# Kernel optimization log

Hardware: AMD Instinct MI355X
Metric: run time of the kernel (lower is better)

Reference implementation:

```python
import jax, jax.numpy as jnp
import numpy as np

NUM_HEADS = 16
HEAD_DIM = 64
EMBED_DIM = 1024
MASKED_BIAS = -10000.0


def setup_inputs() -> dict:
    key = jax.random.key(0)
    ks = jax.random.split(key, 4)
    B, S, D = 4, 1024, EMBED_DIM
    scale = 0.02
    return {
        "hidden_states": jax.random.normal(ks[0], (B, S, D), dtype=jnp.float32),
        "c_attn_w": jax.random.normal(ks[1], (D, 3 * D), dtype=jnp.float32) * scale,
        "c_attn_b": jnp.zeros((3 * D,), dtype=jnp.float32),
        "c_proj_w": jax.random.normal(ks[2], (D, D), dtype=jnp.float32) * scale,
        "c_proj_b": jnp.zeros((D,), dtype=jnp.float32),
        "affine_w": jnp.ones((D,), dtype=jnp.float32),
        "affine_b": jnp.zeros((D,), dtype=jnp.float32),
    }


def reference(hidden_states, c_attn_w, c_attn_b, c_proj_w, c_proj_b, affine_w, affine_b):
    B, S, D = hidden_states.shape
    H, Dh = NUM_HEADS, HEAD_DIM
    # c_attn (GPT2 Conv1D): x @ W + b -> [B,S,3D], split into q,k,v
    qkv = hidden_states @ c_attn_w + c_attn_b
    q, k, v = jnp.split(qkv, 3, axis=-1)
    # split heads -> [B,H,S,Dh]
    def split_heads(t):
        return t.reshape(B, S, H, Dh).transpose(0, 2, 1, 3)
    q, k, v = split_heads(q), split_heads(k), split_heads(v)
    # QK^T scaled by 1/sqrt(head_dim) (value.size(-1)**0.5)
    attn_weights = jnp.einsum("bhqd,bhkd->bhqk", q, k) / jnp.asarray(
        Dh, hidden_states.dtype) ** 0.5
    # causal mask via where with -10000 sentinel (eager GPT2 semantics)
    causal = jnp.tril(jnp.ones((S, S), dtype=bool))[None, None]
    attn_weights = jnp.where(causal, attn_weights,
                             jnp.asarray(MASKED_BIAS, attn_weights.dtype))
    attn_weights = jax.nn.softmax(attn_weights, axis=-1)
    # attn dropout = identity in eval
    attn_output = jnp.einsum("bhqk,bhkd->bhqd", attn_weights, v)
    # merge heads -> [B,S,D]
    attn_output = attn_output.transpose(0, 2, 1, 3).reshape(B, S, D)
    # c_proj (Conv1D), resid dropout identity, then affine
    attn_output = attn_output @ c_proj_w + c_proj_b
    attn_output = attn_output * affine_w + affine_b
    return attn_output
```

## Files before the change

kernel.cpp:

```cpp
#include <hip/hip_runtime.h>


typedef __attribute__((ext_vector_type(4))) float  fx4;
typedef __attribute__((ext_vector_type(4))) short  sx4;
typedef __attribute__((ext_vector_type(8))) short  sx8;
typedef __attribute__((ext_vector_type(4))) float  f32x4;
typedef __attribute__((ext_vector_type(8))) __bf16 bf16x8;

#define DEVI static __device__ __forceinline__

DEVI short f2bf(float f) {
  unsigned u = __builtin_bit_cast(unsigned, f);
  u = (u + 0x7FFFu + ((u >> 16) & 1u)) >> 16;
  return (short)u;
}

DEVI fx4 mfma16(sx8 a, sx8 b, fx4 c) {
  return __builtin_amdgcn_mfma_f32_16x16x32_bf16(
      __builtin_bit_cast(bf16x8, a), __builtin_bit_cast(bf16x8, b), c, 0, 0, 0);
}

DEVI void gl_lds16(const void* g, void* l) {
  __builtin_amdgcn_global_load_lds(
      (const __attribute__((address_space(1))) void*)g,
      (__attribute__((address_space(3))) void*)l, 16, 0, 0);
}

__global__ __launch_bounds__(256) void cast_bf16(const float* __restrict__ in,
                                                 short* __restrict__ out, int n4) {
  int i = blockIdx.x * blockDim.x + threadIdx.x;
  if (i < n4) {
    f32x4 v = *(const f32x4*)&in[(size_t)i * 4];
    sx4 o;
#pragma unroll
    for (int j = 0; j < 4; ++j) o[j] = f2bf(v[j]);
    *(sx4*)&out[(size_t)i * 4] = o;
  }
}

__global__ __launch_bounds__(256) void transpose_bf16(const float* __restrict__ in,
                                                      short* __restrict__ out,
                                                      int R, int C) {
  __shared__ float t[32][33];
  int tx = threadIdx.x & 31, ty = threadIdx.x >> 5;
  int r0 = blockIdx.y * 32, c0 = blockIdx.x * 32;
#pragma unroll
  for (int i = 0; i < 4; ++i)
    t[ty + i * 8][tx] = in[(size_t)(r0 + ty + i * 8) * C + c0 + tx];
  __syncthreads();
#pragma unroll
  for (int i = 0; i < 4; ++i)
    out[(size_t)(c0 + ty + i * 8) * R + r0 + tx] = f2bf(t[tx][ty + i * 8]);
}

__global__ __launch_bounds__(512, 2) void gemm_qkv(
    const short* __restrict__ A, const short* __restrict__ Bt,
    const float* __restrict__ bias, short* __restrict__ Qg,
    short* __restrict__ Kg, short* __restrict__ Vtg) {
  __shared__ __align__(16) short As[2][256][64];
  __shared__ __align__(16) short Bs[2][256][64];
  const int tid = threadIdx.x, lane = tid & 63, w = tid >> 6;
  const int bid = blockIdx.x;
  const int x = bid & 7, k = bid >> 3;
  const int bm = (x & 3) * 4 + (k & 3);
  const int bn = (x >> 2) * 6 + (k >> 2);
  const int wm = w >> 2, wn = w & 3;
  const int c0 = lane & 15, g = lane >> 4;
  const int lr8 = lane >> 3;
  const int ls8 = (lane & 7) ^ lr8;
  const int K = 1024;
  fx4 acc[8][4] = {};

  auto STAGE = [&](int bf, int kt) {
#pragma unroll
    for (int i = 0; i < 4; ++i) {
      int r = w * 32 + i * 8;
      gl_lds16(&A[(size_t)(bm * 256 + r + lr8) * K + kt + ls8 * 8], &As[bf][r][0]);
      gl_lds16(&Bt[(size_t)(bn * 256 + r + lr8) * K + kt + ls8 * 8], &Bs[bf][r][0]);
    }
  };

  STAGE(0, 0);
  for (int t = 0; t < 16; ++t) {
    const int bf = t & 1;
    if (t + 1 < 16) {
      STAGE(bf ^ 1, (t + 1) * 64);
      asm volatile("s_waitcnt vmcnt(8)" ::: "memory");
    } else {
      asm volatile("s_waitcnt vmcnt(0)" ::: "memory");
    }
    __builtin_amdgcn_s_barrier();

#pragma unroll
    for (int q = 0; q < 4; ++q) {
      const int m0 = (q >> 1) * 4, n0 = (q & 1) * 2;
      sx8 af[4][2], bfr[2][2];
#pragma unroll
      for (int m = 0; m < 4; ++m) {
        int row = wm * 128 + (m0 + m) * 16 + c0;
#pragma unroll
        for (int kk = 0; kk < 2; ++kk)
          af[m][kk] = *(const sx8*)&As[bf][row][((kk * 4 + g) ^ (row & 7)) * 8];
      }
#pragma unroll
      for (int n = 0; n < 2; ++n) {
        int row = wn * 64 + (n0 + n) * 16 + c0;
#pragma unroll
        for (int kk = 0; kk < 2; ++kk)
          bfr[n][kk] = *(const sx8*)&Bs[bf][row][((kk * 4 + g) ^ (row & 7)) * 8];
      }
      __builtin_amdgcn_sched_barrier(0);
      __builtin_amdgcn_s_barrier();
      __builtin_amdgcn_s_setprio(1);
#pragma unroll
      for (int kk = 0; kk < 2; ++kk)
#pragma unroll
        for (int m = 0; m < 4; ++m)
#pragma unroll
          for (int n = 0; n < 2; ++n)
            acc[m0 + m][n0 + n] = mfma16(af[m][kk], bfr[n][kk], acc[m0 + m][n0 + n]);
      __builtin_amdgcn_s_setprio(0);
      __builtin_amdgcn_s_barrier();
    }
  }

  const float SCALE_Q = 0.125f * 1.4426950408889634f;
#pragma unroll
  for (int m = 0; m < 8; ++m) {
#pragma unroll
    for (int n = 0; n < 4; ++n) {
      int col = bn * 256 + wn * 64 + n * 16 + c0;
      int row0 = bm * 256 + wm * 128 + m * 16 + g * 4;
      float bv = bias[col];
      int b = row0 >> 10, s0 = row0 & 1023;
      if (col < 1024) {
        int h = col >> 6, d = col & 63;
        size_t base = ((size_t)(b * 16 + h) * 1024) * 64 + d;
#pragma unroll
        for (int r = 0; r < 4; ++r)
          Qg[base + (size_t)(s0 + r) * 64] = f2bf((acc[m][n][r] + bv) * SCALE_Q);
      } else if (col < 2048) {
        int c = col - 1024, h = c >> 6, d = c & 63;
        size_t base = ((size_t)(b * 16 + h) * 1024) * 64 + d;
#pragma unroll
        for (int r = 0; r < 4; ++r)
          Kg[base + (size_t)(s0 + r) * 64] = f2bf(acc[m][n][r] + bv);
      } else {
        int c = col - 2048, h = c >> 6, d = c & 63;
        sx4 v;
#pragma unroll
        for (int r = 0; r < 4; ++r) v[r] = f2bf(acc[m][n][r] + bv);
        *(sx4*)&Vtg[((size_t)(b * 16 + h) * 64 + d) * 1024 + s0] = v;
      }
    }
  }
}

__global__ __launch_bounds__(512, 4) void gemm_proj(
    const short* __restrict__ A, const short* __restrict__ Bt,
    const float* __restrict__ bias, const float* __restrict__ aw,
    const float* __restrict__ ab, float* __restrict__ Out) {
  __shared__ __align__(16) short As[2][128][64];
  __shared__ __align__(16) short Bs[2][128][64];
  const int tid = threadIdx.x, lane = tid & 63, w = tid >> 6;
  const int bid = blockIdx.x;
  const int x = bid & 7, k = bid >> 3;
  const int bn = x + 0 * 8, bm = k;
  const int wm = w >> 2, wn = w & 3;
  const int c0 = lane & 15, g = lane >> 4;
  const int lr8 = lane >> 3, ls8 = (lane & 7) ^ lr8;
  const int K = 1024, N = 1024;
  fx4 acc[4][2] = {};

  auto STAGE = [&](int bf, int kt) {
#pragma unroll
    for (int i = 0; i < 2; ++i) {
      int idx = w * 2 + i;
      gl_lds16(&A[(size_t)(bm * 128 + idx * 8 + lr8) * K + kt + ls8 * 8],
               &As[bf][idx * 8][0]);
      gl_lds16(&Bt[(size_t)(bn * 128 + idx * 8 + lr8) * K + kt + ls8 * 8],
               &Bs[bf][idx * 8][0]);
    }
  };

  STAGE(0, 0);
  for (int t = 0; t < 16; ++t) {
    const int bf = t & 1;
    if (t + 1 < 16) {
      STAGE(bf ^ 1, (t + 1) * 64);
      asm volatile("s_waitcnt vmcnt(4)" ::: "memory");
    } else {
      asm volatile("s_waitcnt vmcnt(0)" ::: "memory");
    }
    __builtin_amdgcn_s_barrier();
    __builtin_amdgcn_s_setprio(1);
#pragma unroll
    for (int kk = 0; kk < 2; ++kk) {
      sx8 af[4], bfr[2];
      int sb = kk * 4 + g;
#pragma unroll
      for (int m = 0; m < 4; ++m) {
        int row = wm * 64 + m * 16 + c0;
        af[m] = *(const sx8*)&As[bf][row][(sb ^ (row & 7)) * 8];
      }
#pragma unroll
      for (int n = 0; n < 2; ++n) {
        int row = wn * 32 + n * 16 + c0;
        bfr[n] = *(const sx8*)&Bs[bf][row][(sb ^ (row & 7)) * 8];
      }
#pragma unroll
      for (int m = 0; m < 4; ++m)
#pragma unroll
        for (int n = 0; n < 2; ++n) acc[m][n] = mfma16(af[m], bfr[n], acc[m][n]);
    }
    __builtin_amdgcn_s_setprio(0);
    __builtin_amdgcn_s_barrier();
  }

#pragma unroll
  for (int m = 0; m < 4; ++m) {
#pragma unroll
    for (int n = 0; n < 2; ++n) {
      int col = bn * 128 + wn * 32 + n * 16 + c0;
      int row0 = bm * 128 + wm * 64 + m * 16 + g * 4;
      float bv = bias[col], wv = aw[col], av = ab[col];
#pragma unroll
      for (int r = 0; r < 4; ++r)
        Out[(size_t)(row0 + r) * N + col] = (acc[m][n][r] + bv) * wv + av;
    }
  }
}

__global__ __launch_bounds__(256, 4) void attn_kernel(const short* __restrict__ Qg,
                                                      const short* __restrict__ Kg,
                                                      const short* __restrict__ Vtg,
                                                      short* __restrict__ AO) {
  __shared__ __align__(16) short Ks[2][64][64];
  __shared__ __align__(16) short Vts[2][64][64];
  __shared__ __align__(16) short Ps[4][16 * 64];
  const int tid = threadIdx.x, lane = tid & 63, w = tid >> 6;
  const int bid = blockIdx.x;
  const int u = bid >> 8, v = bid & 255, bh = v >> 2, jj = v & 3;
  const int qt = (u == 0) ? jj : (u == 1) ? 7 - jj : (u == 2) ? 8 + jj : 15 - jj;
  const int b = bh >> 4, h = bh & 15;
  const int c0 = lane & 15, g = lane >> 4;
  const int lr8 = lane >> 3, ls8 = (lane & 7) ^ lr8;
  const int q0 = qt * 64 + w * 16;
  const short* Qp = Qg + (size_t)bh * 65536;
  const short* Kp = Kg + (size_t)bh * 65536;
  const short* Vp = Vtg + (size_t)bh * 65536;
  short* pbase = &Ps[w][0];
  const int s8 = (c0 & 7) * 8;

  sx8 qf[2];
#pragma unroll
  for (int kk = 0; kk < 2; ++kk)
    qf[kk] = *(const sx8*)&Qp[(size_t)(q0 + c0) * 64 + kk * 32 + g * 8];

  fx4 o[4] = {};
  float mrun = -1e30f, lrun = 0.f;
  const int q_glob = q0 + c0;

  auto STAGE = [&](int bf, int kv0) {
#pragma unroll
    for (int i = 0; i < 2; ++i) {
      int idx = w * 2 + i;
      gl_lds16(&Kp[(size_t)(kv0 + idx * 8 + lr8) * 64 + ls8 * 8], &Ks[bf][idx * 8][0]);
    }
#pragma unroll
    for (int i = 0; i < 2; ++i) {
      int idx = w * 2 + i;
      gl_lds16(&Vp[(size_t)(idx * 8 + lr8) * 1024 + kv0 + ls8 * 8], &Vts[bf][idx * 8][0]);
    }
  };

  STAGE(0, 0);
  for (int t = 0; t <= qt; ++t) {
    const int kv0 = t * 64;
    const int bf = t & 1;
    const bool more = t < qt;
    if (more) {
      STAGE(bf ^ 1, kv0 + 64);
      asm volatile("s_waitcnt vmcnt(4)" ::: "memory");
    } else {
      asm volatile("s_waitcnt vmcnt(0)" ::: "memory");
    }
    __builtin_amdgcn_s_barrier();

    fx4 st[4];
    __builtin_amdgcn_s_setprio(1);
#pragma unroll
    for (int mf = 0; mf < 4; ++mf) {
      int row = mf * 16 + c0;
      sx8 kf0 = *(const sx8*)&Ks[bf][row][(g ^ (row & 7)) * 8];
      sx8 kf1 = *(const sx8*)&Ks[bf][row][((4 + g) ^ (row & 7)) * 8];
      fx4 z = {0.f, 0.f, 0.f, 0.f};
      z = mfma16(kf0, qf[0], z);
      st[mf] = mfma16(kf1, qf[1], z);
    }
    __builtin_amdgcn_s_setprio(0);

    float pmax = -1e30f;
    if (t == qt) {
#pragma unroll
      for (int mf = 0; mf < 4; ++mf)
#pragma unroll
        for (int r = 0; r < 4; ++r) {
          int kv = kv0 + mf * 16 + g * 4 + r;
          float z = (kv > q_glob) ? -1e30f : st[mf][r];
          st[mf][r] = z;
          pmax = fmaxf(pmax, z);
        }
    } else {
#pragma unroll
      for (int mf = 0; mf < 4; ++mf)
#pragma unroll
        for (int r = 0; r < 4; ++r) pmax = fmaxf(pmax, st[mf][r]);
    }
    pmax = fmaxf(pmax, __shfl_xor(pmax, 16));
    pmax = fmaxf(pmax, __shfl_xor(pmax, 32));
    float mnew = fmaxf(mrun, pmax);
    float alpha = __builtin_amdgcn_exp2f(mrun - mnew);
    float psum = 0.f;
#pragma unroll
    for (int mf = 0; mf < 4; ++mf) {
      sx4 pv;
#pragma unroll
      for (int r = 0; r < 4; ++r) {
        float pp = __builtin_amdgcn_exp2f(st[mf][r] - mnew);
        psum += pp;
        pv[r] = f2bf(pp);
      }
      *(sx4*)&pbase[c0 * 64 + ((mf * 16 + g * 4) ^ s8)] = pv;
    }
    psum += __shfl_xor(psum, 16);
    psum += __shfl_xor(psum, 32);
    lrun = lrun * alpha + psum;
    mrun = mnew;
#pragma unroll
    for (int mf = 0; mf < 4; ++mf) o[mf] *= alpha;

    __builtin_amdgcn_s_setprio(1);
#pragma unroll
    for (int kk = 0; kk < 2; ++kk) {
      sx8 pbf = *(const sx8*)&pbase[c0 * 64 + ((kk * 32 + g * 8) ^ s8)];
#pragma unroll
      for (int mf = 0; mf < 4; ++mf) {
        int row = mf * 16 + c0;
        sx8 vaf = *(const sx8*)&Vts[bf][row][((kk * 4 + g) ^ (row & 7)) * 8];
        o[mf] = mfma16(vaf, pbf, o[mf]);
      }
    }
    __builtin_amdgcn_s_setprio(0);
    __builtin_amdgcn_s_barrier();
  }

  float inv = 1.0f / lrun;
  int q = q0 + c0;
#pragma unroll
  for (int mf = 0; mf < 4; ++mf) {
    sx4 v4;
#pragma unroll
    for (int r = 0; r < 4; ++r) v4[r] = f2bf(o[mf][r] * inv);
    int d0 = mf * 16 + g * 4;
    *(sx4*)&AO[((size_t)(b * 1024 + q)) * 1024 + h * 64 + d0] = v4;
  }
}

extern "C" void kernel_launch(void* const* d_in, const int* in_sizes, int n_in,
                              void* d_out, int out_size, void* d_ws, size_t ws_size,
                              hipStream_t stream) {
  const float* hs  = (const float*)d_in[0];
  const float* caw = (const float*)d_in[1];
  const float* cab = (const float*)d_in[2];
  const float* cpw = (const float*)d_in[3];
  const float* cpb = (const float*)d_in[4];
  const float* afw = (const float*)d_in[5];
  const float* afb = (const float*)d_in[6];
  float* out = (float*)d_out;
  char* ws = (char*)d_ws;

  short* hsb    = (short*)(ws);
  short* ao     = (short*)(ws);
  short* wqkvt  = (short*)(ws + ((size_t)8  << 20));
  short* wprojt = (short*)(ws + ((size_t)14 << 20));
  short* Qg     = (short*)(ws + ((size_t)16 << 20));
  short* Kg     = (short*)(ws + ((size_t)24 << 20));
  short* Vtg    = (short*)(ws + ((size_t)32 << 20));

  cast_bf16<<<4096, 256, 0, stream>>>(hs, hsb, 1048576);
  transpose_bf16<<<dim3(96, 32), 256, 0, stream>>>(caw, wqkvt, 1024, 3072);
  transpose_bf16<<<dim3(32, 32), 256, 0, stream>>>(cpw, wprojt, 1024, 1024);
  gemm_qkv<<<192, 512, 0, stream>>>(hsb, wqkvt, cab, Qg, Kg, Vtg);
  attn_kernel<<<1024, 256, 0, stream>>>(Qg, Kg, Vtg, ao);
  gemm_proj<<<256, 512, 0, stream>>>(ao, wprojt, cpb, afw, afb, out);
}
```

Before: 110.6 us.

## Halve QKV GEMM K-tile to 32 and drop intra-tile quadrant barriers

The QKV GEMM now stages K-slices of 32 instead of 64, halving LDS use per buffer, and uses a new XOR swizzle suited to 4 slots per row. The main loop runs 32 iterations, each loading all 8x4 fragments at once and issuing 32 MFMAs with a single barrier, instead of four quadrant phases separated by extra barriers. This is meant to cut synchronisation overhead and LDS footprint, possibly raising occupancy. In exchange it doubles the number of global-load stages and barriers per tile and raises fragment register pressure.

```diff
diff --git a/kernel.cpp b/kernel.cpp
--- a/kernel.cpp
+++ b/kernel.cpp
@@ -57,8 +57,8 @@
     const short* __restrict__ A, const short* __restrict__ Bt,
     const float* __restrict__ bias, short* __restrict__ Qg,
     short* __restrict__ Kg, short* __restrict__ Vtg) {
-  __shared__ __align__(16) short As[2][256][64];
-  __shared__ __align__(16) short Bs[2][256][64];
+  __shared__ __align__(16) short As[2][256][32];
+  __shared__ __align__(16) short Bs[2][256][32];
   const int tid = threadIdx.x, lane = tid & 63, w = tid >> 6;
   const int bid = blockIdx.x;
   const int x = bid & 7, k = bid >> 3;
@@ -66,62 +66,51 @@
   const int bn = (x >> 2) * 6 + (k >> 2);
   const int wm = w >> 2, wn = w & 3;
   const int c0 = lane & 15, g = lane >> 4;
-  const int lr8 = lane >> 3;
-  const int ls8 = (lane & 7) ^ lr8;
+  const int lr16 = lane >> 2;
+  const int xs = (lr16 ^ (lr16 >> 2)) & 3;
+  const int src_slot = (lane & 3) ^ xs;
   const int K = 1024;
   fx4 acc[8][4] = {};
 
   auto STAGE = [&](int bf, int kt) {
 #pragma unroll
-    for (int i = 0; i < 4; ++i) {
-      int r = w * 32 + i * 8;
-      gl_lds16(&A[(size_t)(bm * 256 + r + lr8) * K + kt + ls8 * 8], &As[bf][r][0]);
-      gl_lds16(&Bt[(size_t)(bn * 256 + r + lr8) * K + kt + ls8 * 8], &Bs[bf][r][0]);
+    for (int i = 0; i < 2; ++i) {
+      int ch = w * 2 + i;
+      int row = ch * 16 + lr16;
+      gl_lds16(&A[(size_t)(bm * 256 + row) * K + kt + src_slot * 8], &As[bf][ch * 16][0]);
+      gl_lds16(&Bt[(size_t)(bn * 256 + row) * K + kt + src_slot * 8], &Bs[bf][ch * 16][0]);
     }
   };
 
   STAGE(0, 0);
-  for (int t = 0; t < 16; ++t) {
+  for (int t = 0; t < 32; ++t) {
     const int bf = t & 1;
-    if (t + 1 < 16) {
-      STAGE(bf ^ 1, (t + 1) * 64);
-      asm volatile("s_waitcnt vmcnt(8)" ::: "memory");
+    if (t + 1 < 32) {
+      STAGE(bf ^ 1, (t + 1) * 32);
+      asm volatile("s_waitcnt vmcnt(4)" ::: "memory");
     } else {
       asm volatile("s_waitcnt vmcnt(0)" ::: "memory");
     }
     __builtin_amdgcn_s_barrier();
 
-#pragma unroll
-    for (int q = 0; q < 4; ++q) {
-      const int m0 = (q >> 1) * 4, n0 = (q & 1) * 2;
-      sx8 af[4][2], bfr[2][2];
-#pragma unroll
-      for (int m = 0; m < 4; ++m) {
-        int row = wm * 128 + (m0 + m) * 16 + c0;
-#pragma unroll
-        for (int kk = 0; kk < 2; ++kk)
-          af[m][kk] = *(const sx8*)&As[bf][row][((kk * 4 + g) ^ (row & 7)) * 8];
-      }
-#pragma unroll
-      for (int n = 0; n < 2; ++n) {
-        int row = wn * 64 + (n0 + n) * 16 + c0;
-#pragma unroll
-        for (int kk = 0; kk < 2; ++kk)
-          bfr[n][kk] = *(const sx8*)&Bs[bf][row][((kk * 4 + g) ^ (row & 7)) * 8];
-      }
-      __builtin_amdgcn_sched_barrier(0);
-      __builtin_amdgcn_s_barrier();
-      __builtin_amdgcn_s_setprio(1);
-#pragma unroll
-      for (int kk = 0; kk < 2; ++kk)
-#pragma unroll
-        for (int m = 0; m < 4; ++m)
-#pragma unroll
-          for (int n = 0; n < 2; ++n)
-            acc[m0 + m][n0 + n] = mfma16(af[m][kk], bfr[n][kk], acc[m0 + m][n0 + n]);
-      __builtin_amdgcn_s_setprio(0);
-      __builtin_amdgcn_s_barrier();
-    }
+    sx8 af[8], bfr[4];
+#pragma unroll
+    for (int m = 0; m < 8; ++m) {
+      int row = wm * 128 + m * 16 + c0;
+      af[m] = *(const sx8*)&As[bf][row][(g ^ ((row ^ (row >> 2)) & 3)) * 8];
+    }
+#pragma unroll
+    for (int n = 0; n < 4; ++n) {
+      int row = wn * 64 + n * 16 + c0;
+      bfr[n] = *(const sx8*)&Bs[bf][row][(g ^ ((row ^ (row >> 2)) & 3)) * 8];
+    }
+    __builtin_amdgcn_s_setprio(1);
+#pragma unroll
+    for (int m = 0; m < 8; ++m)
+#pragma unroll
+      for (int n = 0; n < 4; ++n) acc[m][n] = mfma16(af[m], bfr[n], acc[m][n]);
+    __builtin_amdgcn_s_setprio(0);
+    __builtin_amdgcn_s_barrier();
   }
 
   const float SCALE_Q = 0.125f * 1.4426950408889634f;
@@ -165,7 +154,7 @@
   const int tid = threadIdx.x, lane = tid & 63, w = tid >> 6;
   const int bid = blockIdx.x;
   const int x = bid & 7, k = bid >> 3;
-  const int bn = x + 0 * 8, bm = k;
+  const int bn = x, bm = k;
   const int wm = w >> 2, wn = w & 3;
   const int c0 = lane & 15, g = lane >> 4;
   const int lr8 = lane >> 3, ls8 = (lane & 7) ^ lr8;
```

Result: no change. 110.0 us (-0.6%).

## Restructure QKV GEMM into 4-phase half-tile pipeline with interleaved loads

Applied to the files above, without the earlier changes.

The QKV GEMM main loop is rewritten so that A and B tiles are staged in halves, one half at a time, and each half-load is issued between MFMA phases. Fragments are reused across quadrants (af reused for two n-halves, bfr kept for all four), which cuts LDS reads. Loads run up to two k-steps ahead, so global-to-LDS traffic overlaps with compute more finely. The cost is more barriers per iteration and more complex vmcnt accounting, plus a higher risk of a race between half-tile writes and reads. Barriers in the other kernels are switched to an inline asm s_barrier with a memory clobber.

```diff
diff --git a/kernel.cpp b/kernel.cpp
--- a/kernel.cpp
+++ b/kernel.cpp
@@ -8,6 +8,7 @@
 typedef __attribute__((ext_vector_type(8))) __bf16 bf16x8;
 
 #define DEVI static __device__ __forceinline__
+#define BARRIER asm volatile("s_barrier" ::: "memory")
 
 DEVI short f2bf(float f) {
   unsigned u = __builtin_bit_cast(unsigned, f);
@@ -66,62 +67,122 @@
   const int bn = (x >> 2) * 6 + (k >> 2);
   const int wm = w >> 2, wn = w & 3;
   const int c0 = lane & 15, g = lane >> 4;
-  const int lr8 = lane >> 3;
-  const int ls8 = (lane & 7) ^ lr8;
+  const int lr8 = lane >> 3, ls8 = (lane & 7) ^ lr8;
   const int K = 1024;
+  const int sw = c0 & 7;
   fx4 acc[8][4] = {};
 
-  auto STAGE = [&](int bf, int kt) {
-#pragma unroll
-    for (int i = 0; i < 4; ++i) {
-      int r = w * 32 + i * 8;
-      gl_lds16(&A[(size_t)(bm * 256 + r + lr8) * K + kt + ls8 * 8], &As[bf][r][0]);
-      gl_lds16(&Bt[(size_t)(bn * 256 + r + lr8) * K + kt + ls8 * 8], &Bs[bf][r][0]);
+  auto SA = [&](int h, int u) {
+    if (u > 15) return;
+    const int bf = u & 1;
+#pragma unroll
+    for (int i = 0; i < 2; ++i) {
+      int ch = w * 2 + i;
+      int r = (ch >> 3) * 128 + h * 64 + (ch & 7) * 8;
+      gl_lds16(&A[(size_t)(bm * 256 + r + lr8) * K + u * 64 + ls8 * 8],
+               &As[bf][r][0]);
     }
   };
-
-  STAGE(0, 0);
+  auto SB = [&](int h, int u) {
+    if (u > 15) return;
+    const int bf = u & 1;
+#pragma unroll
+    for (int i = 0; i < 2; ++i) {
+      int ch = w * 2 + i;
+      int r = (ch >> 2) * 64 + h * 32 + (ch & 3) * 8;
+      gl_lds16(&Bt[(size_t)(bn * 256 + r + lr8) * K + u * 64 + ls8 * 8],
+               &Bs[bf][r][0]);
+    }
+  };
+
+  SA(0, 0); SB(0, 0); SA(1, 0); SB(1, 0); SA(0, 1); SB(0, 1);
+  asm volatile("s_waitcnt vmcnt(0)" ::: "memory");
+  BARRIER;
+
+  sx8 af[4][2], bfr[4][2];
   for (int t = 0; t < 16; ++t) {
     const int bf = t & 1;
-    if (t + 1 < 16) {
-      STAGE(bf ^ 1, (t + 1) * 64);
-      asm volatile("s_waitcnt vmcnt(8)" ::: "memory");
-    } else {
+#pragma unroll
+    for (int mi = 0; mi < 4; ++mi) {
+      int r = wm * 128 + mi * 16 + c0;
+#pragma unroll
+      for (int kk = 0; kk < 2; ++kk)
+        af[mi][kk] = *(const sx8*)&As[bf][r][(((kk << 2) | g) ^ sw) * 8];
+    }
+#pragma unroll
+    for (int n = 0; n < 2; ++n) {
+      int r = wn * 64 + n * 16 + c0;
+#pragma unroll
+      for (int kk = 0; kk < 2; ++kk)
+        bfr[n][kk] = *(const sx8*)&Bs[bf][r][(((kk << 2) | g) ^ sw) * 8];
+    }
+    SA(1, t + 1);
+    BARRIER;
+    __builtin_amdgcn_s_setprio(1);
+#pragma unroll
+    for (int kk = 0; kk < 2; ++kk)
+#pragma unroll
+      for (int mi = 0; mi < 4; ++mi)
+#pragma unroll
+        for (int n = 0; n < 2; ++n)
+          acc[mi][n] = mfma16(af[mi][kk], bfr[n][kk], acc[mi][n]);
+    __builtin_amdgcn_s_setprio(0);
+    BARRIER;
+#pragma unroll
+    for (int n = 2; n < 4; ++n) {
+      int r = wn * 64 + n * 16 + c0;
+#pragma unroll
+      for (int kk = 0; kk < 2; ++kk)
+        bfr[n][kk] = *(const sx8*)&Bs[bf][r][(((kk << 2) | g) ^ sw) * 8];
+    }
+    SB(1, t + 1);
+    BARRIER;
+    __builtin_amdgcn_s_setprio(1);
+#pragma unroll
+    for (int kk = 0; kk < 2; ++kk)
+#pragma unroll
+      for (int mi = 0; mi < 4; ++mi)
+#pragma unroll
+        for (int n = 2; n < 4; ++n)
+          acc[mi][n] = mfma16(af[mi][kk], bfr[n][kk], acc[mi][n]);
+    __builtin_amdgcn_s_setprio(0);
+    BARRIER;
+#pragma unroll
+    for (int mi = 0; mi < 4; ++mi) {
+      int r = wm * 128 + 64 + mi * 16 + c0;
+#pragma unroll
+      for (int kk = 0; kk < 2; ++kk)
+        af[mi][kk] = *(const sx8*)&As[bf][r][(((kk << 2) | g) ^ sw) * 8];
+    }
+    SA(0, t + 2);
+    BARRIER;
+    __builtin_amdgcn_s_setprio(1);
+#pragma unroll
+    for (int kk = 0; kk < 2; ++kk)
+#pragma unroll
+      for (int mi = 0; mi < 4; ++mi)
+#pragma unroll
+        for (int n = 2; n < 4; ++n)
+          acc[4 + mi][n] = mfma16(af[mi][kk], bfr[n][kk], acc[4 + mi][n]);
+    __builtin_amdgcn_s_setprio(0);
+    BARRIER;
+    SB(0, t + 2);
+    if (t < 14) {
+      asm volatile("s_waitcnt vmcnt(4)" ::: "memory");
+    } else if (t == 14) {
       asm volatile("s_waitcnt vmcnt(0)" ::: "memory");
     }
-    __builtin_amdgcn_s_barrier();
-
-#pragma unroll
-    for (int q = 0; q < 4; ++q) {
-      const int m0 = (q >> 1) * 4, n0 = (q & 1) * 2;
-      sx8 af[4][2], bfr[2][2];
-#pragma unroll
-      for (int m = 0; m < 4; ++m) {
-        int row = wm * 128 + (m0 + m) * 16 + c0;
-#pragma unroll
-        for (int kk = 0; kk < 2; ++kk)
-          af[m][kk] = *(const sx8*)&As[bf][row][((kk * 4 + g) ^ (row & 7)) * 8];
-      }
-#pragma unroll
-      for (int n = 0; n < 2; ++n) {
-        int row = wn * 64 + (n0 + n) * 16 + c0;
-#pragma unroll
-        for (int kk = 0; kk < 2; ++kk)
-          bfr[n][kk] = *(const sx8*)&Bs[bf][row][((kk * 4 + g) ^ (row & 7)) * 8];
-      }
-      __builtin_amdgcn_sched_barrier(0);
-      __builtin_amdgcn_s_barrier();
-      __builtin_amdgcn_s_setprio(1);
-#pragma unroll
-      for (int kk = 0; kk < 2; ++kk)
-#pragma unroll
-        for (int m = 0; m < 4; ++m)
-#pragma unroll
-          for (int n = 0; n < 2; ++n)
-            acc[m0 + m][n0 + n] = mfma16(af[m][kk], bfr[n][kk], acc[m0 + m][n0 + n]);
-      __builtin_amdgcn_s_setprio(0);
-      __builtin_amdgcn_s_barrier();
-    }
+    BARRIER;
+    __builtin_amdgcn_s_setprio(1);
+#pragma unroll
+    for (int kk = 0; kk < 2; ++kk)
+#pragma unroll
+      for (int mi = 0; mi < 4; ++mi)
+#pragma unroll
+        for (int n = 0; n < 2; ++n)
+          acc[4 + mi][n] = mfma16(af[mi][kk], bfr[n][kk], acc[4 + mi][n]);
+    __builtin_amdgcn_s_setprio(0);
+    BARRIER;
   }
 
   const float SCALE_Q = 0.125f * 1.4426950408889634f;
@@ -165,7 +226,7 @@
   const int tid = threadIdx.x, lane = tid & 63, w = tid >> 6;
   const int bid = blockIdx.x;
   const int x = bid & 7, k = bid >> 3;
-  const int bn = x + 0 * 8, bm = k;
+  const int bn = x, bm = k;
   const int wm = w >> 2, wn = w & 3;
   const int c0 = lane & 15, g = lane >> 4;
   const int lr8 = lane >> 3, ls8 = (lane & 7) ^ lr8;
@@ -192,7 +253,7 @@
     } else {
       asm volatile("s_waitcnt vmcnt(0)" ::: "memory");
     }
-    __builtin_amdgcn_s_barrier();
+    BARRIER;
     __builtin_amdgcn_s_setprio(1);
 #pragma unroll
     for (int kk = 0; kk < 2; ++kk) {
@@ -214,7 +275,7 @@
         for (int n = 0; n < 2; ++n) acc[m][n] = mfma16(af[m], bfr[n], acc[m][n]);
     }
     __builtin_amdgcn_s_setprio(0);
-    __builtin_amdgcn_s_barrier();
+    BARRIER;
   }
 
 #pragma unroll
@@ -285,7 +346,7 @@
     } else {
       asm volatile("s_waitcnt vmcnt(0)" ::: "memory");
     }
-    __builtin_amdgcn_s_barrier();
+    BARRIER;
 
     fx4 st[4];
     __builtin_amdgcn_s_setprio(1);
@@ -352,7 +413,7 @@
       }
     }
     __builtin_amdgcn_s_setprio(0);
-    __builtin_amdgcn_s_barrier();
+    BARRIER;
   }
 
   float inv = 1.0f / lrun;
```

After: 97.57 us. 1.13x faster.
